# Kernel optimization log

Hardware: AMD Instinct MI355X
Metric: run time of the kernel (lower is better)

Reference implementation:

```python
import jax, jax.numpy as jnp
import numpy as np

N_EMB = 1024
N_HEAD = 16
HD = N_EMB // N_HEAD
ROPE_BASE = 10000.0


def _rope_cos_sin(seq_len, dim, dtype):
    inv_freq = 1.0 / (ROPE_BASE ** (jnp.arange(0, dim, 2, dtype=jnp.float32) / dim))
    t = jnp.arange(seq_len, dtype=jnp.float32)
    freqs = jnp.outer(t, inv_freq)              # [S, dim/2]
    emb = jnp.concatenate([freqs, freqs], -1)    # [S, dim]
    return jnp.cos(emb).astype(dtype), jnp.sin(emb).astype(dtype)


def _rotate_half(x):
    x1, x2 = jnp.split(x, 2, axis=-1)
    return jnp.concatenate([-x2, x1], axis=-1)


def _apply_rope(x):
    # x: [B, H, L, hd]; rotary over sequence axis (-2)
    cos, sin = _rope_cos_sin(x.shape[-2], x.shape[-1], x.dtype)
    return x * cos + _rotate_half(x) * sin


def setup_inputs() -> dict:
    key = jax.random.key(0)
    ks = jax.random.split(key, 8)
    B, T, S = 2, 2048, 2048
    std = 0.02
    return {
        "x": jax.random.normal(ks[0], (B, T, N_EMB), jnp.float32),
        "memory": jax.random.normal(ks[1], (B, S, N_EMB), jnp.float32),
        "q_w": jax.random.normal(ks[2], (N_EMB, N_EMB), jnp.float32) * std,
        "q_b": jnp.zeros((N_EMB,), jnp.float32),
        "kv_w": jax.random.normal(ks[3], (N_EMB, 2 * N_EMB), jnp.float32) * std,
        "kv_b": jnp.zeros((2 * N_EMB,), jnp.float32),
        "proj_w": jax.random.normal(ks[4], (N_EMB, N_EMB), jnp.float32) * std,
        "proj_b": jnp.zeros((N_EMB,), jnp.float32),
    }


def reference(x, memory, q_w, q_b, kv_w, kv_b, proj_w, proj_b):
    B, S, C = memory.shape
    T = x.shape[1]
    kv = memory @ kv_w + kv_b                      # [B,S,2C]
    K, V = jnp.split(kv, 2, axis=-1)
    Q = x @ q_w + q_b                              # [B,T,C]

    def heads(t, L):
        return t.reshape(B, L, N_HEAD, HD).transpose(0, 2, 1, 3)

    Q, K, V = heads(Q, T), heads(K, S), heads(V, S)
    Q = jax.nn.elu(Q) + 1.0                        # positive feature map
    K = jax.nn.elu(K) + 1.0
    Q_rot = _apply_rope(Q)
    K_rot = _apply_rope(K)
    # denom row-sum: sum_s Q.K_s == Q . (sum_s K_s) -- identical math, no SxT matrix
    denom = jnp.einsum('bhtd,bhd->bht', Q, K.sum(axis=2))[..., None]  # [B,H,T,1]
    att = jnp.einsum('bhtd,bhsd->bhts', Q_rot, K_rot) / denom          # [B,H,T,S]
    y = jnp.einsum('bhts,bhsd->bhtd', att, V)                          # [B,H,T,hd]
    y = y.transpose(0, 2, 1, 3).reshape(B, T, C)
    return y @ proj_w + proj_b
```

## Files before the change

kernel.cpp:

```cpp
#include <hip/hip_runtime.h>
#include <cstddef>
#include <cstdint>

#define B_SZ  2
#define T_SEQ 2048
#define S_SEQ 2048
#define C_EMB 1024
#define NH    16
#define HD    64
#define KDIM  1024

typedef __attribute__((ext_vector_type(8))) short bf16x8;
typedef __attribute__((ext_vector_type(4))) float f32x4;

#define OFF_XH    ((size_t)0)
#define OFF_XL    ((size_t)2097152)
#define OFF_MEMH  ((size_t)4194304)
#define OFF_MEML  ((size_t)6291456)
#define OFF_QWH   ((size_t)8388608)
#define OFF_QWL   ((size_t)8912896)
#define OFF_KVWH  ((size_t)9437184)
#define OFF_KVWL  ((size_t)10485760)
#define OFF_PWH   ((size_t)11534336)
#define OFF_PWL   ((size_t)12058624)
#define OFF_KSUM  ((size_t)12582912)
#define OFF_MT    ((size_t)12584960)
#define OFF_TAB   ((size_t)12716032)
#define OFF_YH    ((size_t)12847104)
#define OFF_YL    ((size_t)14944256)
#define WS_FLOATS ((size_t)17041408)

__device__ __forceinline__ float elu1(float v) {
    return v > 0.0f ? v + 1.0f : __expf(v);
}
__device__ __forceinline__ unsigned short bf16_rne(float x) {
    union { float f; unsigned int u; } v; v.f = x;
    unsigned int u = v.u;
    return (unsigned short)((u + 0x7FFFu + ((u >> 16) & 1u)) >> 16);
}
__device__ __forceinline__ float bf16_to_f(unsigned short h) {
    union { unsigned int u; float f; } v; v.u = ((unsigned int)h) << 16;
    return v.f;
}

#define PREP_BLOCKS 13064

__device__ __forceinline__ void split4_body(
    const float4* __restrict__ in, ushort4* __restrict__ hi,
    ushort4* __restrict__ lo, int i)
{
    float4 v = in[i];
    ushort4 h, l;
    h.x = bf16_rne(v.x); l.x = bf16_rne(v.x - bf16_to_f(h.x));
    h.y = bf16_rne(v.y); l.y = bf16_rne(v.y - bf16_to_f(h.y));
    h.z = bf16_rne(v.z); l.z = bf16_rne(v.z - bf16_to_f(h.z));
    h.w = bf16_rne(v.w); l.w = bf16_rne(v.w - bf16_to_f(h.w));
    hi[i] = h; lo[i] = l;
}

__device__ __forceinline__ void transpose_body(
    const float* __restrict__ W, unsigned short* __restrict__ Wth,
    unsigned short* __restrict__ Wtl, int K, int N, int bx, int by,
    float (*tile)[33])
{
    const int k0 = by * 32, n0 = bx * 32;
    const int tx = threadIdx.x & 31, ty = threadIdx.x >> 5;
    #pragma unroll
    for (int j = 0; j < 4; ++j)
        tile[ty + j * 8][tx] = W[(size_t)(k0 + ty + j * 8) * N + n0 + tx];
    __syncthreads();
    #pragma unroll
    for (int j = 0; j < 4; ++j) {
        float x = tile[tx][ty + j * 8];
        unsigned short h = bf16_rne(x);
        unsigned short l = bf16_rne(x - bf16_to_f(h));
        size_t o = (size_t)(n0 + ty + j * 8) * K + k0 + tx;
        Wth[o] = h; Wtl[o] = l;
    }
}

__global__ __launch_bounds__(256) void prep_kernel(
    const float* __restrict__ x, const float* __restrict__ memory,
    const float* __restrict__ q_w, const float* __restrict__ kv_w,
    const float* __restrict__ proj_w,
    unsigned short* __restrict__ xh, unsigned short* __restrict__ xl,
    unsigned short* __restrict__ mh, unsigned short* __restrict__ ml,
    unsigned short* __restrict__ qwh, unsigned short* __restrict__ qwl,
    unsigned short* __restrict__ kvwh, unsigned short* __restrict__ kvwl,
    unsigned short* __restrict__ pwh, unsigned short* __restrict__ pwl,
    float2* __restrict__ tab, float* __restrict__ zero_base)
{
    __shared__ float tile[32][33];
    const int bid = blockIdx.x;
    const int tid = threadIdx.x;
    if (bid < 4096) {
        split4_body((const float4*)x, (ushort4*)xh, (ushort4*)xl, bid * 256 + tid);
    } else if (bid < 8192) {
        split4_body((const float4*)memory, (ushort4*)mh, (ushort4*)ml, (bid - 4096) * 256 + tid);
    } else if (bid < 9216) {
        int i = bid - 8192;
        transpose_body(q_w, qwh, qwl, 1024, 1024, i & 31, i >> 5, tile);
    } else if (bid < 11264) {
        int i = bid - 9216;
        transpose_body(kv_w, kvwh, kvwl, 1024, 2048, i & 63, i >> 6, tile);
    } else if (bid < 12288) {
        int i = bid - 11264;
        transpose_body(proj_w, pwh, pwl, 1024, 1024, i & 31, i >> 5, tile);
    } else if (bid < 12544) {
        int idx = (bid - 12288) * 256 + tid;
        int pos = idx >> 5, i = idx & 31;
        double invf = exp(-(double)i * (9.210340371976184 / 32.0));
        float arg = (float)((double)pos * invf);
        float sn, cs;
        sincosf(arg, &sn, &cs);
        tab[idx] = make_float2(cs, sn);
    } else {
        int idx = (bid - 12544) * 256 + tid;
        if (idx < 2048 + 131072) zero_base[idx] = 0.0f;
    }
}

#define WAITCNT_VM(N)   asm volatile("s_waitcnt vmcnt(" #N ")" ::: "memory")
#define WAITCNT_LGKM(N) asm volatile("s_waitcnt lgkmcnt(" #N ")" ::: "memory")
#define CBAR()          asm volatile("" ::: "memory")

__device__ __forceinline__ void xcd_swz16(int& bx, int& by) {
    int id = (int)(blockIdx.x + (blockIdx.y << 4));
    int x = id & 7, k = id >> 3;
    bx = k >> 1;
    by = x * 2 + (k & 1);
}
__device__ __forceinline__ void xcd_swz32(int& bx, int& by) {
    int id = (int)(blockIdx.x + (blockIdx.y << 4));
    int x = id & 7, k = id >> 3;
    bx = k >> 2;
    by = x * 4 + (k & 3);
}

__global__ __launch_bounds__(512, 2) void gemm_kv(
    const unsigned short* __restrict__ Ah, const unsigned short* __restrict__ Al,
    const unsigned short* __restrict__ Bth, const unsigned short* __restrict__ Btl,
    const float* __restrict__ bias, const float2* __restrict__ tab,
    float* __restrict__ Ksum, float* __restrict__ Mt)
{
    __shared__ alignas(16) unsigned short smem[67584];
    const int tid = threadIdx.x;
    const int w = tid >> 6, lane = tid & 63;
    const int wr = w >> 1, wc = w & 1;
    const int quad = lane >> 4, lrow = lane & 15;
    int h, mt;
    xcd_swz16(h, mt);
    const int m0 = mt * 256;
    const int n0 = h * 64;
    const int b  = m0 >> 11;
    const int tbase = (m0 & 2047) + wr * 64;
    const int bh_idx = b * NH + h;

    const int sr = tid >> 2;
    const int g  = (tid & 3) ^ ((tid >> 3) & 3);
    const unsigned short* gA0 = Ah + (size_t)(m0 + sr) * KDIM + g * 8;
    const unsigned short* gA1 = Ah + (size_t)(m0 + 128 + sr) * KDIM + g * 8;
    const unsigned short* gA2 = Al + (size_t)(m0 + sr) * KDIM + g * 8;
    const unsigned short* gA3 = Al + (size_t)(m0 + 128 + sr) * KDIM + g * 8;
    const size_t brow = (size_t)(n0 + sr) + (sr >= 64 ? (size_t)960 : 0);
    const unsigned short* gB0 = Bth + brow * KDIM + g * 8;
    const unsigned short* gB1 = Btl + brow * KDIM + g * 8;
    const int lA0 = w * 512;
    const int lA1 = 4096 + w * 512;
    const int lA2 = 8192 + w * 512;
    const int lA3 = 12288 + w * 512;
    const int lB0 = 16384 + w * 512;
    const int lB1 = 20480 + w * 512;

    auto STAGE = [&](unsigned short* buf, int k0) {
        __builtin_amdgcn_global_load_lds(
            (const __attribute__((address_space(1))) unsigned int*)(gA0 + k0),
            (__attribute__((address_space(3))) unsigned int*)(buf + lA0), 16, 0, 0);
        __builtin_amdgcn_global_load_lds(
            (const __attribute__((address_space(1))) unsigned int*)(gA1 + k0),
            (__attribute__((address_space(3))) unsigned int*)(buf + lA1), 16, 0, 0);
        __builtin_amdgcn_global_load_lds(
            (const __attribute__((address_space(1))) unsigned int*)(gA2 + k0),
            (__attribute__((address_space(3))) unsigned int*)(buf + lA2), 16, 0, 0);
        __builtin_amdgcn_global_load_lds(
            (const __attribute__((address_space(1))) unsigned int*)(gA3 + k0),
            (__attribute__((address_space(3))) unsigned int*)(buf + lA3), 16, 0, 0);
        __builtin_amdgcn_global_load_lds(
            (const __attribute__((address_space(1))) unsigned int*)(gB0 + k0),
            (__attribute__((address_space(3))) unsigned int*)(buf + lB0), 16, 0, 0);
        __builtin_amdgcn_global_load_lds(
            (const __attribute__((address_space(1))) unsigned int*)(gB1 + k0),
            (__attribute__((address_space(3))) unsigned int*)(buf + lB1), 16, 0, 0);
    };

    const int rowbase = wr * 64, colbase = wc * 64;
    const int sw = ((quad ^ ((lrow >> 1) & 3)) << 3);

    f32x4 acc[4][4] = {};
    bf16x8 ahA[4], alA[4], bhA[4], blA[4];
    bf16x8 ahB[4], alB[4], bhB[4], blB[4];

    auto KV_READ = [&](bf16x8 (&AH)[4], bf16x8 (&AL)[4],
                       bf16x8 (&BH)[4], bf16x8 (&BL)[4],
                       const unsigned short* _b) {
        #pragma unroll
        for (int it = 0; it < 4; ++it) {
            int off = (rowbase + it * 16 + lrow) * 32 + sw;
            AH[it] = *(const bf16x8*)&_b[off];
            AL[it] = *(const bf16x8*)&_b[8192 + off];
        }
        #pragma unroll
        for (int jt = 0; jt < 4; ++jt) {
            int boff = (colbase + jt * 16 + lrow) * 32 + sw;
            BH[jt] = *(const bf16x8*)&_b[16384 + boff];
            BL[jt] = *(const bf16x8*)&_b[20480 + boff];
        }
    };
    auto KV_MFMA = [&](bf16x8 (&AH)[4], bf16x8 (&AL)[4],
                       bf16x8 (&BH)[4], bf16x8 (&BL)[4]) {
        #pragma unroll
        for (int it = 0; it < 4; ++it)
            #pragma unroll
            for (int jt = 0; jt < 4; ++jt)
                acc[it][jt] = __builtin_amdgcn_mfma_f32_16x16x32_bf16(AH[it], BH[jt], acc[it][jt], 0, 0, 0);
        #pragma unroll
        for (int it = 0; it < 4; ++it)
            #pragma unroll
            for (int jt = 0; jt < 4; ++jt)
                acc[it][jt] = __builtin_amdgcn_mfma_f32_16x16x32_bf16(AH[it], BL[jt], acc[it][jt], 0, 0, 0);
        #pragma unroll
        for (int it = 0; it < 4; ++it)
            #pragma unroll
            for (int jt = 0; jt < 4; ++jt)
                acc[it][jt] = __builtin_amdgcn_mfma_f32_16x16x32_bf16(AL[it], BH[jt], acc[it][jt], 0, 0, 0);
    };

    unsigned short* buf0 = smem;
    unsigned short* buf1 = smem + 24576;

    STAGE(buf0, 0);
    STAGE(buf1, 32);
    WAITCNT_VM(6);
    __builtin_amdgcn_s_barrier();
    KV_READ(ahA, alA, bhA, blA, buf0);

    #pragma unroll 1
    for (int t = 0; t < 32; t += 2) {
        WAITCNT_VM(0);
        WAITCNT_LGKM(0);
        __builtin_amdgcn_sched_barrier(0);
        __builtin_amdgcn_s_barrier();
        __builtin_amdgcn_sched_barrier(0);
        if (t + 2 < 32) STAGE(buf0, (t + 2) * 32);
        KV_READ(ahB, alB, bhB, blB, buf1);
        __builtin_amdgcn_s_setprio(1);
        KV_MFMA(ahA, alA, bhA, blA);
        __builtin_amdgcn_s_setprio(0);

        WAITCNT_VM(0);
        WAITCNT_LGKM(0);
        __builtin_amdgcn_sched_barrier(0);
        __builtin_amdgcn_s_barrier();
        __builtin_amdgcn_sched_barrier(0);
        if (t + 3 < 32) STAGE(buf1, (t + 3) * 32);
        if (t + 2 < 32) KV_READ(ahA, alA, bhA, blA, buf0);
        __builtin_amdgcn_s_setprio(1);
        KV_MFMA(ahB, alB, bhB, blB);
        __builtin_amdgcn_s_setprio(0);
    }
    __syncthreads();

    const bool isK = (wc == 0);
    const int colg = (isK ? 0 : C_EMB) + h * 64;
    float bb[4];
    #pragma unroll
    for (int jt = 0; jt < 4; ++jt) bb[jt] = bias[colg + jt * 16 + lrow];
    #pragma unroll
    for (int it = 0; it < 4; ++it)
        #pragma unroll
        for (int jt = 0; jt < 4; ++jt)
            #pragma unroll
            for (int r = 0; r < 4; ++r) {
                float v = acc[it][jt][r] + bb[jt];
                acc[it][jt][r] = isK ? elu1(v) : v;
            }

    if (isK) {
        #pragma unroll
        for (int jt = 0; jt < 4; ++jt) {
            float p = 0.0f;
            #pragma unroll
            for (int it = 0; it < 4; ++it)
                #pragma unroll
                for (int r = 0; r < 4; ++r) p += acc[it][jt][r];
            p += __shfl_xor(p, 16);
            p += __shfl_xor(p, 32);
            if (quad == 0)
                atomicAdd(&Ksum[b * C_EMB + h * 64 + jt * 16 + lrow], p);
        }
        #pragma unroll
        for (int it = 0; it < 4; ++it)
            #pragma unroll
            for (int r = 0; r < 4; ++r) {
                int s = tbase + it * 16 + quad * 4 + r;
                float2 c0 = tab[s * 32 + lrow];
                float2 c1 = tab[s * 32 + 16 + lrow];
                float a0 = acc[it][0][r], a1 = acc[it][1][r];
                float a2 = acc[it][2][r], a3 = acc[it][3][r];
                acc[it][0][r] = a0 * c0.x - a2 * c0.y;
                acc[it][2][r] = a2 * c0.x + a0 * c0.y;
                acc[it][1][r] = a1 * c1.x - a3 * c1.y;
                acc[it][3][r] = a3 * c1.x + a1 * c1.y;
            }
    }

    unsigned short* Hd = smem + (isK ? 0 : 33792);
    unsigned short* Ld = Hd + 16896;
    #pragma unroll
    for (int jt = 0; jt < 4; ++jt) {
        int d = jt * 16 + lrow;
        #pragma unroll
        for (int it = 0; it < 4; ++it) {
            int t0loc = wr * 64 + it * 16 + quad * 4;
            ushort4 h4, l4;
            float v0 = acc[it][jt][0], v1 = acc[it][jt][1];
            float v2 = acc[it][jt][2], v3 = acc[it][jt][3];
            h4.x = bf16_rne(v0); l4.x = bf16_rne(v0 - bf16_to_f(h4.x));
            h4.y = bf16_rne(v1); l4.y = bf16_rne(v1 - bf16_to_f(h4.y));
            h4.z = bf16_rne(v2); l4.z = bf16_rne(v2 - bf16_to_f(h4.z));
            h4.w = bf16_rne(v3); l4.w = bf16_rne(v3 - bf16_to_f(h4.w));
            *(ushort4*)&Hd[d * 264 + t0loc] = h4;
            *(ushort4*)&Ld[d * 264 + t0loc] = l4;
        }
    }
    __syncthreads();

    {
        const unsigned short* KH = smem;
        const unsigned short* KL = smem + 16896;
        const unsigned short* VH = smem + 33792;
        const unsigned short* VL = smem + 50688;
        const int mrow = (w & 3) * 16 + lrow;
        const int thalf = w >> 2;
        f32x4 macc[4] = {};
        #pragma unroll
        for (int ks = 0; ks < 4; ++ks) {
            int kof = thalf * 128 + ks * 32 + quad * 8;
            bf16x8 vah = *(const bf16x8*)&VH[mrow * 264 + kof];
            bf16x8 val = *(const bf16x8*)&VL[mrow * 264 + kof];
            #pragma unroll
            for (int jt = 0; jt < 4; ++jt) {
                int nrow = jt * 16 + lrow;
                bf16x8 kbh = *(const bf16x8*)&KH[nrow * 264 + kof];
                bf16x8 kbl = *(const bf16x8*)&KL[nrow * 264 + kof];
                macc[jt] = __builtin_amdgcn_mfma_f32_16x16x32_bf16(vah, kbh, macc[jt], 0, 0, 0);
                macc[jt] = __builtin_amdgcn_mfma_f32_16x16x32_bf16(vah, kbl, macc[jt], 0, 0, 0);
                macc[jt] = __builtin_amdgcn_mfma_f32_16x16x32_bf16(val, kbh, macc[jt], 0, 0, 0);
            }
        }
        #pragma unroll
        for (int jt = 0; jt < 4; ++jt)
            #pragma unroll
            for (int r = 0; r < 4; ++r)
                atomicAdd(&Mt[((size_t)bh_idx * 64 + (w & 3) * 16 + quad * 4 + r) * 64 + jt * 16 + lrow],
                          macc[jt][r]);
    }
}

__device__ __forceinline__ void gemm_main_128(
    const unsigned short* __restrict__ Ah, const unsigned short* __restrict__ Al,
    const unsigned short* __restrict__ Bth, const unsigned short* __restrict__ Btl,
    unsigned short* lds, int m0, int n0, f32x4 (&acc)[2][4])
{
    const int tid = threadIdx.x;
    const int w = tid >> 6, lane = tid & 63;
    const int quad = lane >> 4, lrow = lane & 15;
    const int srow = lane >> 2;
    const int g  = (lane & 3) ^ ((lane >> 3) & 3);
    const int sw = ((quad ^ ((lrow >> 1) & 3)) << 3);

    const unsigned short* gA0 = Ah + (size_t)(m0 + w * 16 + srow) * KDIM + g * 8;
    const unsigned short* gA1 = Ah + (size_t)(m0 + 64 + w * 16 + srow) * KDIM + g * 8;
    const unsigned short* gA2 = Al + (size_t)(m0 + w * 16 + srow) * KDIM + g * 8;
    const unsigned short* gA3 = Al + (size_t)(m0 + 64 + w * 16 + srow) * KDIM + g * 8;
    const unsigned short* gB0 = Bth + (size_t)(n0 + w * 16 + srow) * KDIM + g * 8;
    const unsigned short* gB1 = Btl + (size_t)(n0 + w * 16 + srow) * KDIM + g * 8;
    const int lA0 = w * 512, lA1 = 2048 + w * 512;
    const int lA2 = 4096 + w * 512, lA3 = 6144 + w * 512;
    const int lB0 = 8192 + w * 512, lB1 = 10240 + w * 512;

    auto STAGE = [&](unsigned short* buf, int k0) {
        __builtin_amdgcn_global_load_lds(
            (const __attribute__((address_space(1))) unsigned int*)(gA0 + k0),
            (__attribute__((address_space(3))) unsigned int*)(buf + lA0), 16, 0, 0);
        __builtin_amdgcn_global_load_lds(
            (const __attribute__((address_space(1))) unsigned int*)(gA1 + k0),
            (__attribute__((address_space(3))) unsigned int*)(buf + lA1), 16, 0, 0);
        __builtin_amdgcn_global_load_lds(
            (const __attribute__((address_space(1))) unsigned int*)(gA2 + k0),
            (__attribute__((address_space(3))) unsigned int*)(buf + lA2), 16, 0, 0);
        __builtin_amdgcn_global_load_lds(
            (const __attribute__((address_space(1))) unsigned int*)(gA3 + k0),
            (__attribute__((address_space(3))) unsigned int*)(buf + lA3), 16, 0, 0);
        __builtin_amdgcn_global_load_lds(
            (const __attribute__((address_space(1))) unsigned int*)(gB0 + k0),
            (__attribute__((address_space(3))) unsigned int*)(buf + lB0), 16, 0, 0);
        __builtin_amdgcn_global_load_lds(
            (const __attribute__((address_space(1))) unsigned int*)(gB1 + k0),
            (__attribute__((address_space(3))) unsigned int*)(buf + lB1), 16, 0, 0);
    };

    STAGE(lds, 0);

    #pragma unroll 1
    for (int t = 0; t < 32; ++t) {
        unsigned short* cur = lds + (t & 1) * 12288;
        unsigned short* nxt = lds + ((t + 1) & 1) * 12288;
        WAITCNT_VM(0);
        __builtin_amdgcn_sched_barrier(0);
        __builtin_amdgcn_s_barrier();
        __builtin_amdgcn_sched_barrier(0);

        bf16x8 ah[2], al[2], bh[4], bl[4];
        #pragma unroll
        for (int it = 0; it < 2; ++it) {
            int off = (w * 32 + it * 16 + lrow) * 32 + sw;
            ah[it] = *(const bf16x8*)&cur[off];
            al[it] = *(const bf16x8*)&cur[4096 + off];
        }
        #pragma unroll
        for (int jt = 0; jt < 2; ++jt) {
            int boff = (jt * 16 + lrow) * 32 + sw;
            bh[jt] = *(const bf16x8*)&cur[8192 + boff];
            bl[jt] = *(const bf16x8*)&cur[10240 + boff];
        }
        CBAR();
        #pragma unroll
        for (int jt = 2; jt < 4; ++jt) {
            int boff = (jt * 16 + lrow) * 32 + sw;
            bh[jt] = *(const bf16x8*)&cur[8192 + boff];
            bl[jt] = *(const bf16x8*)&cur[10240 + boff];
        }
        if (t + 1 < 32) STAGE(nxt, (t + 1) * 32);

        WAITCNT_LGKM(4);
        __builtin_amdgcn_sched_barrier(0);
        __builtin_amdgcn_s_setprio(1);
        #pragma unroll
        for (int it = 0; it < 2; ++it)
            #pragma unroll
            for (int jt = 0; jt < 2; ++jt)
                acc[it][jt] = __builtin_amdgcn_mfma_f32_16x16x32_bf16(ah[it], bh[jt], acc[it][jt], 0, 0, 0);
        #pragma unroll
        for (int it = 0; it < 2; ++it)
            #pragma unroll
            for (int jt = 0; jt < 2; ++jt)
                acc[it][jt] = __builtin_amdgcn_mfma_f32_16x16x32_bf16(ah[it], bl[jt], acc[it][jt], 0, 0, 0);
        #pragma unroll
        for (int it = 0; it < 2; ++it)
            #pragma unroll
            for (int jt = 0; jt < 2; ++jt)
                acc[it][jt] = __builtin_amdgcn_mfma_f32_16x16x32_bf16(al[it], bh[jt], acc[it][jt], 0, 0, 0);

        WAITCNT_LGKM(0);
        __builtin_amdgcn_sched_barrier(0);
        #pragma unroll
        for (int it = 0; it < 2; ++it)
            #pragma unroll
            for (int jt = 2; jt < 4; ++jt)
                acc[it][jt] = __builtin_amdgcn_mfma_f32_16x16x32_bf16(ah[it], bh[jt], acc[it][jt], 0, 0, 0);
        #pragma unroll
        for (int it = 0; it < 2; ++it)
            #pragma unroll
            for (int jt = 2; jt < 4; ++jt)
                acc[it][jt] = __builtin_amdgcn_mfma_f32_16x16x32_bf16(ah[it], bl[jt], acc[it][jt], 0, 0, 0);
        #pragma unroll
        for (int it = 0; it < 2; ++it)
            #pragma unroll
            for (int jt = 2; jt < 4; ++jt)
                acc[it][jt] = __builtin_amdgcn_mfma_f32_16x16x32_bf16(al[it], bh[jt], acc[it][jt], 0, 0, 0);
        __builtin_amdgcn_s_setprio(0);
    }
    __syncthreads();
}

__global__ __launch_bounds__(256, 3) void gemm_q(
    const unsigned short* __restrict__ Ah, const unsigned short* __restrict__ Al,
    const unsigned short* __restrict__ Bth, const unsigned short* __restrict__ Btl,
    const float* __restrict__ bias, const float2* __restrict__ tab,
    const float* __restrict__ Ksum, const float* __restrict__ Mt,
    unsigned short* __restrict__ Yh, unsigned short* __restrict__ Yl)
{
    __shared__ alignas(16) unsigned short smem[24576];
    int h, mt;
    xcd_swz32(h, mt);
    const int m0 = mt * 128;
    f32x4 acc[2][4] = {};
    gemm_main_128(Ah, Al, Bth, Btl, smem, m0, h * 64, acc);

    const int tid = threadIdx.x;
    const int w = tid >> 6, lane = tid & 63;
    const int quad = lane >> 4, lrow = lane & 15;
    const int b = m0 >> 11;
    const int tbase = (m0 & 2047) + w * 32;
    const int bh = b * NH + h;

    float bb[4];
    #pragma unroll
    for (int jt = 0; jt < 4; ++jt) bb[jt] = bias[h * 64 + jt * 16 + lrow];
    #pragma unroll
    for (int it = 0; it < 2; ++it)
        #pragma unroll
        for (int jt = 0; jt < 4; ++jt)
            #pragma unroll
            for (int r = 0; r < 4; ++r)
                acc[it][jt][r] = elu1(acc[it][jt][r] + bb[jt]);

    float ks[4], den_reg[2][4];
    #pragma unroll
    for (int jt = 0; jt < 4; ++jt) ks[jt] = Ksum[b * C_EMB + h * 64 + jt * 16 + lrow];
    #pragma unroll
    for (int it = 0; it < 2; ++it)
        #pragma unroll
        for (int r = 0; r < 4; ++r) {
            float p = acc[it][0][r] * ks[0] + acc[it][1][r] * ks[1]
                    + acc[it][2][r] * ks[2] + acc[it][3][r] * ks[3];
            p += __shfl_xor(p, 1);
            p += __shfl_xor(p, 2);
            p += __shfl_xor(p, 4);
            p += __shfl_xor(p, 8);
            den_reg[it][r] = p;
        }

    #pragma unroll
    for (int it = 0; it < 2; ++it)
        #pragma unroll
        for (int r = 0; r < 4; ++r) {
            int s = tbase + it * 16 + quad * 4 + r;
            float2 c0 = tab[s * 32 + lrow];
            float2 c1 = tab[s * 32 + 16 + lrow];
            float a0 = acc[it][0][r], a1 = acc[it][1][r];
            float a2 = acc[it][2][r], a3 = acc[it][3][r];
            acc[it][0][r] = a0 * c0.x - a2 * c0.y;
            acc[it][2][r] = a2 * c0.x + a0 * c0.y;
            acc[it][1][r] = a1 * c1.x - a3 * c1.y;
            acc[it][3][r] = a3 * c1.x + a1 * c1.y;
        }

    unsigned short* QH = smem + w * 4608;
    unsigned short* QL = QH + 2304;
    #pragma unroll
    for (int it = 0; it < 2; ++it)
        #pragma unroll
        for (int jt = 0; jt < 4; ++jt)
            #pragma unroll
            for (int r = 0; r < 4; ++r) {
                int tloc = it * 16 + quad * 4 + r;
                int d = jt * 16 + lrow;
                float v = acc[it][jt][r];
                unsigned short hh = bf16_rne(v);
                QH[tloc * 72 + d] = hh;
                QL[tloc * 72 + d] = bf16_rne(v - bf16_to_f(hh));
            }

    f32x4 acc2[2][4] = {};
    #pragma unroll
    for (int kc = 0; kc < 2; ++kc) {
        bf16x8 mbh[4], mbl[4];
        #pragma unroll
        for (int jt2 = 0; jt2 < 4; ++jt2) {
            const float* mp = &Mt[((size_t)bh * 64 + jt2 * 16 + lrow) * 64 + kc * 32 + quad * 8];
            #pragma unroll
            for (int e = 0; e < 8; ++e) {
                float x = mp[e];
                unsigned short hh = bf16_rne(x);
                mbh[jt2][e] = (short)hh;
                mbl[jt2][e] = (short)bf16_rne(x - bf16_to_f(hh));
            }
        }
        #pragma unroll
        for (int it2 = 0; it2 < 2; ++it2) {
            int ro = (it2 * 16 + lrow) * 72 + kc * 32 + quad * 8;
            bf16x8 qh = *(const bf16x8*)&QH[ro];
            bf16x8 ql = *(const bf16x8*)&QL[ro];
            #pragma unroll
            for (int jt2 = 0; jt2 < 4; ++jt2) {
                acc2[it2][jt2] = __builtin_amdgcn_mfma_f32_16x16x32_bf16(qh, mbh[jt2], acc2[it2][jt2], 0, 0, 0);
                acc2[it2][jt2] = __builtin_amdgcn_mfma_f32_16x16x32_bf16(qh, mbl[jt2], acc2[it2][jt2], 0, 0, 0);
                acc2[it2][jt2] = __builtin_amdgcn_mfma_f32_16x16x32_bf16(ql, mbh[jt2], acc2[it2][jt2], 0, 0, 0);
            }
        }
    }

    #pragma unroll
    for (int it2 = 0; it2 < 2; ++it2)
        #pragma unroll
        for (int jt2 = 0; jt2 < 4; ++jt2)
            #pragma unroll
            for (int r = 0; r < 4; ++r) {
                float v = acc2[it2][jt2][r] / den_reg[it2][r];
                size_t o = ((size_t)(m0 + w * 32 + it2 * 16 + quad * 4 + r)) * C_EMB
                         + h * 64 + jt2 * 16 + lrow;
                unsigned short hh = bf16_rne(v);
                Yh[o] = hh;
                Yl[o] = bf16_rne(v - bf16_to_f(hh));
            }
}

__global__ __launch_bounds__(256, 3) void gemm_out(
    const unsigned short* __restrict__ Ah, const unsigned short* __restrict__ Al,
    const unsigned short* __restrict__ Bth, const unsigned short* __restrict__ Btl,
    const float* __restrict__ bias, float* __restrict__ out)
{
    __shared__ alignas(16) unsigned short smem[24576];
    int nt, mt;
    xcd_swz32(nt, mt);
    const int m0 = mt * 128, n0 = nt * 64;
    f32x4 acc[2][4] = {};
    gemm_main_128(Ah, Al, Bth, Btl, smem, m0, n0, acc);

    const int tid = threadIdx.x;
    const int w = tid >> 6, lane = tid & 63;
    const int quad = lane >> 4, lrow = lane & 15;

    #pragma unroll
    for (int jt = 0; jt < 4; ++jt) {
        int gc = n0 + jt * 16 + lrow;
        float bb = bias[gc];
        #pragma unroll
        for (int it = 0; it < 2; ++it) {
            int grb = m0 + w * 32 + it * 16 + quad * 4;
            #pragma unroll
            for (int r = 0; r < 4; ++r)
                out[(size_t)(grb + r) * C_EMB + gc] = acc[it][jt][r] + bb;
        }
    }
}

extern "C" void kernel_launch(void* const* d_in, const int* in_sizes, int n_in,
                              void* d_out, int out_size, void* d_ws, size_t ws_size,
                              hipStream_t stream)
{
    const float* x      = (const float*)d_in[0];
    const float* memory = (const float*)d_in[1];
    const float* q_w    = (const float*)d_in[2];
    const float* q_b    = (const float*)d_in[3];
    const float* kv_w   = (const float*)d_in[4];
    const float* kv_b   = (const float*)d_in[5];
    const float* proj_w = (const float*)d_in[6];
    const float* proj_b = (const float*)d_in[7];

    if (ws_size < WS_FLOATS * sizeof(float)) return;

    float* ws = (float*)d_ws;
    unsigned short* xh   = (unsigned short*)(ws + OFF_XH);
    unsigned short* xl   = (unsigned short*)(ws + OFF_XL);
    unsigned short* mh   = (unsigned short*)(ws + OFF_MEMH);
    unsigned short* ml   = (unsigned short*)(ws + OFF_MEML);
    unsigned short* qwh  = (unsigned short*)(ws + OFF_QWH);
    unsigned short* qwl  = (unsigned short*)(ws + OFF_QWL);
    unsigned short* kvwh = (unsigned short*)(ws + OFF_KVWH);
    unsigned short* kvwl = (unsigned short*)(ws + OFF_KVWL);
    unsigned short* pwh  = (unsigned short*)(ws + OFF_PWH);
    unsigned short* pwl  = (unsigned short*)(ws + OFF_PWL);
    unsigned short* Yh   = (unsigned short*)(ws + OFF_YH);
    unsigned short* Yl   = (unsigned short*)(ws + OFF_YL);
    float*  Ksum = ws + OFF_KSUM;
    float*  Mm   = ws + OFF_MT;
    float2* tab  = (float2*)(ws + OFF_TAB);

    prep_kernel<<<PREP_BLOCKS, 256, 0, stream>>>(
        x, memory, q_w, kv_w, proj_w,
        xh, xl, mh, ml, qwh, qwl, kvwh, kvwl, pwh, pwl,
        tab, Ksum );

    gemm_kv<<<dim3(16, 16), 512, 0, stream>>>(mh, ml, kvwh, kvwl, kv_b, tab, Ksum, Mm);
    gemm_q<<<dim3(16, 32), 256, 0, stream>>>(xh, xl, qwh, qwl, q_b, tab, Ksum, Mm, Yh, Yl);
    gemm_out<<<dim3(16, 32), 256, 0, stream>>>(Yh, Yl, pwh, pwl, proj_b, (float*)d_out);
}
```

Baseline: 242.9 us.

## Halve gemm_kv M-tile to 128 rows and restructure its double-buffered pipeline

Changes the KV projection kernel from 256-row to 128-row tiles, doubling the grid to 512 blocks and raising launch bounds to allow 4 blocks per CU with half the LDS. The K-loop is rewritten to a single-step double buffer that splits the B-fragment reads and MFMAs into two halves, with partial lgkm waits. The aim is better occupancy and CU coverage, at the cost of lower per-block data reuse and twice as many atomic adds into Ksum and Mt.

```diff
diff --git a/kernel.cpp b/kernel.cpp
--- a/kernel.cpp
+++ b/kernel.cpp
@@ -124,12 +124,6 @@
 #define WAITCNT_LGKM(N) asm volatile("s_waitcnt lgkmcnt(" #N ")" ::: "memory")
 #define CBAR()          asm volatile("" ::: "memory")
 
-__device__ __forceinline__ void xcd_swz16(int& bx, int& by) {
-    int id = (int)(blockIdx.x + (blockIdx.y << 4));
-    int x = id & 7, k = id >> 3;
-    bx = k >> 1;
-    by = x * 2 + (k & 1);
-}
 __device__ __forceinline__ void xcd_swz32(int& bx, int& by) {
     int id = (int)(blockIdx.x + (blockIdx.y << 4));
     int x = id & 7, k = id >> 3;
@@ -137,135 +131,127 @@
     by = x * 4 + (k & 3);
 }
 
-__global__ __launch_bounds__(512, 2) void gemm_kv(
+__global__ __launch_bounds__(512, 4) void gemm_kv(
     const unsigned short* __restrict__ Ah, const unsigned short* __restrict__ Al,
     const unsigned short* __restrict__ Bth, const unsigned short* __restrict__ Btl,
     const float* __restrict__ bias, const float2* __restrict__ tab,
     float* __restrict__ Ksum, float* __restrict__ Mt)
 {
-    __shared__ alignas(16) unsigned short smem[67584];
+    __shared__ alignas(16) unsigned short smem[34816];
     const int tid = threadIdx.x;
     const int w = tid >> 6, lane = tid & 63;
     const int wr = w >> 1, wc = w & 1;
     const int quad = lane >> 4, lrow = lane & 15;
     int h, mt;
-    xcd_swz16(h, mt);
-    const int m0 = mt * 256;
+    xcd_swz32(h, mt);
+    const int m0 = mt * 128;
     const int n0 = h * 64;
     const int b  = m0 >> 11;
-    const int tbase = (m0 & 2047) + wr * 64;
+    const int tbase = (m0 & 2047) + wr * 32;
     const int bh_idx = b * NH + h;
 
-    const int sr = tid >> 2;
-    const int g  = (tid & 3) ^ ((tid >> 3) & 3);
-    const unsigned short* gA0 = Ah + (size_t)(m0 + sr) * KDIM + g * 8;
-    const unsigned short* gA1 = Ah + (size_t)(m0 + 128 + sr) * KDIM + g * 8;
-    const unsigned short* gA2 = Al + (size_t)(m0 + sr) * KDIM + g * 8;
-    const unsigned short* gA3 = Al + (size_t)(m0 + 128 + sr) * KDIM + g * 8;
-    const size_t brow = (size_t)(n0 + sr) + (sr >= 64 ? (size_t)960 : 0);
-    const unsigned short* gB0 = Bth + brow * KDIM + g * 8;
-    const unsigned short* gB1 = Btl + brow * KDIM + g * 8;
-    const int lA0 = w * 512;
-    const int lA1 = 4096 + w * 512;
-    const int lA2 = 8192 + w * 512;
-    const int lA3 = 12288 + w * 512;
-    const int lB0 = 16384 + w * 512;
-    const int lB1 = 20480 + w * 512;
+    const int sr = lane >> 2;
+    const int g  = (lane & 3) ^ ((lane >> 3) & 3);
+    const int arow = w * 16 + sr;
+    const unsigned short* gAh = Ah + (size_t)(m0 + arow) * KDIM + g * 8;
+    const unsigned short* gAl = Al + (size_t)(m0 + arow) * KDIM + g * 8;
+    const size_t brow = (size_t)(n0 + arow) + ((w >= 4) ? (size_t)960 : 0);
+    const unsigned short* gBh = Bth + brow * KDIM + g * 8;
+    const unsigned short* gBl = Btl + brow * KDIM + g * 8;
+    const int lAh = w * 512;
+    const int lAl = 4096 + w * 512;
+    const int lBh = 8192 + w * 512;
+    const int lBl = 12288 + w * 512;
 
     auto STAGE = [&](unsigned short* buf, int k0) {
         __builtin_amdgcn_global_load_lds(
-            (const __attribute__((address_space(1))) unsigned int*)(gA0 + k0),
-            (__attribute__((address_space(3))) unsigned int*)(buf + lA0), 16, 0, 0);
-        __builtin_amdgcn_global_load_lds(
-            (const __attribute__((address_space(1))) unsigned int*)(gA1 + k0),
-            (__attribute__((address_space(3))) unsigned int*)(buf + lA1), 16, 0, 0);
-        __builtin_amdgcn_global_load_lds(
-            (const __attribute__((address_space(1))) unsigned int*)(gA2 + k0),
-            (__attribute__((address_space(3))) unsigned int*)(buf + lA2), 16, 0, 0);
-        __builtin_amdgcn_global_load_lds(
-            (const __attribute__((address_space(1))) unsigned int*)(gA3 + k0),
-            (__attribute__((address_space(3))) unsigned int*)(buf + lA3), 16, 0, 0);
-        __builtin_amdgcn_global_load_lds(
-            (const __attribute__((address_space(1))) unsigned int*)(gB0 + k0),
-            (__attribute__((address_space(3))) unsigned int*)(buf + lB0), 16, 0, 0);
-        __builtin_amdgcn_global_load_lds(
-            (const __attribute__((address_space(1))) unsigned int*)(gB1 + k0),
-            (__attribute__((address_space(3))) unsigned int*)(buf + lB1), 16, 0, 0);
+            (const __attribute__((address_space(1))) unsigned int*)(gAh + k0),
+            (__attribute__((address_space(3))) unsigned int*)(buf + lAh), 16, 0, 0);
+        __builtin_amdgcn_global_load_lds(
+            (const __attribute__((address_space(1))) unsigned int*)(gAl + k0),
+            (__attribute__((address_space(3))) unsigned int*)(buf + lAl), 16, 0, 0);
+        __builtin_amdgcn_global_load_lds(
+            (const __attribute__((address_space(1))) unsigned int*)(gBh + k0),
+            (__attribute__((address_space(3))) unsigned int*)(buf + lBh), 16, 0, 0);
+        __builtin_amdgcn_global_load_lds(
+            (const __attribute__((address_space(1))) unsigned int*)(gBl + k0),
+            (__attribute__((address_space(3))) unsigned int*)(buf + lBl), 16, 0, 0);
     };
 
-    const int rowbase = wr * 64, colbase = wc * 64;
+    const int rowbase = wr * 32, colbase = wc * 64;
     const int sw = ((quad ^ ((lrow >> 1) & 3)) << 3);
 
-    f32x4 acc[4][4] = {};
-    bf16x8 ahA[4], alA[4], bhA[4], blA[4];
-    bf16x8 ahB[4], alB[4], bhB[4], blB[4];
-
-    auto KV_READ = [&](bf16x8 (&AH)[4], bf16x8 (&AL)[4],
-                       bf16x8 (&BH)[4], bf16x8 (&BL)[4],
-                       const unsigned short* _b) {
-        #pragma unroll
-        for (int it = 0; it < 4; ++it) {
+    f32x4 acc[2][4] = {};
+
+    STAGE(smem, 0);
+
+    #pragma unroll 1
+    for (int t = 0; t < 32; ++t) {
+        unsigned short* cur = smem + (t & 1) * 16384;
+        unsigned short* nxt = smem + ((t + 1) & 1) * 16384;
+        WAITCNT_VM(0);
+        __builtin_amdgcn_sched_barrier(0);
+        __builtin_amdgcn_s_barrier();
+        __builtin_amdgcn_sched_barrier(0);
+
+        bf16x8 ah[2], al[2], bh[4], bl[4];
+        #pragma unroll
+        for (int it = 0; it < 2; ++it) {
             int off = (rowbase + it * 16 + lrow) * 32 + sw;
-            AH[it] = *(const bf16x8*)&_b[off];
-            AL[it] = *(const bf16x8*)&_b[8192 + off];
-        }
-        #pragma unroll
-        for (int jt = 0; jt < 4; ++jt) {
+            ah[it] = *(const bf16x8*)&cur[off];
+            al[it] = *(const bf16x8*)&cur[4096 + off];
+        }
+        #pragma unroll
+        for (int jt = 0; jt < 2; ++jt) {
             int boff = (colbase + jt * 16 + lrow) * 32 + sw;
-            BH[jt] = *(const bf16x8*)&_b[16384 + boff];
-            BL[jt] = *(const bf16x8*)&_b[20480 + boff];
-        }
-    };
-    auto KV_MFMA = [&](bf16x8 (&AH)[4], bf16x8 (&AL)[4],
-                       bf16x8 (&BH)[4], bf16x8 (&BL)[4]) {
-        #pragma unroll
-        for (int it = 0; it < 4; ++it)
-            #pragma unroll
-            for (int jt = 0; jt < 4; ++jt)
-                acc[it][jt] = __builtin_amdgcn_mfma_f32_16x16x32_bf16(AH[it], BH[jt], acc[it][jt], 0, 0, 0);
-        #pragma unroll
-        for (int it = 0; it < 4; ++it)
-            #pragma unroll
-            for (int jt = 0; jt < 4; ++jt)
-                acc[it][jt] = __builtin_amdgcn_mfma_f32_16x16x32_bf16(AH[it], BL[jt], acc[it][jt], 0, 0, 0);
-        #pragma unroll
-        for (int it = 0; it < 4; ++it)
-            #pragma unroll
-            for (int jt = 0; jt < 4; ++jt)
-                acc[it][jt] = __builtin_amdgcn_mfma_f32_16x16x32_bf16(AL[it], BH[jt], acc[it][jt], 0, 0, 0);
-    };
-
-    unsigned short* buf0 = smem;
-    unsigned short* buf1 = smem + 24576;
-
-    STAGE(buf0, 0);
-    STAGE(buf1, 32);
-    WAITCNT_VM(6);
-    __builtin_amdgcn_s_barrier();
-    KV_READ(ahA, alA, bhA, blA, buf0);
-
-    #pragma unroll 1
-    for (int t = 0; t < 32; t += 2) {
-        WAITCNT_VM(0);
+            bh[jt] = *(const bf16x8*)&cur[8192 + boff];
+            bl[jt] = *(const bf16x8*)&cur[12288 + boff];
+        }
+        CBAR();
+        #pragma unroll
+        for (int jt = 2; jt < 4; ++jt) {
+            int boff = (colbase + jt * 16 + lrow) * 32 + sw;
+            bh[jt] = *(const bf16x8*)&cur[8192 + boff];
+            bl[jt] = *(const bf16x8*)&cur[12288 + boff];
+        }
+        if (t + 1 < 32) STAGE(nxt, (t + 1) * 32);
+
+        WAITCNT_LGKM(4);
+        __builtin_amdgcn_sched_barrier(0);
+        __builtin_amdgcn_s_setprio(1);
+        #pragma unroll
+        for (int it = 0; it < 2; ++it)
+            #pragma unroll
+            for (int jt = 0; jt < 2; ++jt)
+                acc[it][jt] = __builtin_amdgcn_mfma_f32_16x16x32_bf16(ah[it], bh[jt], acc[it][jt], 0, 0, 0);
+        #pragma unroll
+        for (int it = 0; it < 2; ++it)
+            #pragma unroll
+            for (int jt = 0; jt < 2; ++jt)
+                acc[it][jt] = __builtin_amdgcn_mfma_f32_16x16x32_bf16(ah[it], bl[jt], acc[it][jt], 0, 0, 0);
+        #pragma unroll
+        for (int it = 0; it < 2; ++it)
+            #pragma unroll
+            for (int jt = 0; jt < 2; ++jt)
+                acc[it][jt] = __builtin_amdgcn_mfma_f32_16x16x32_bf16(al[it], bh[jt], acc[it][jt], 0, 0, 0);
+
         WAITCNT_LGKM(0);
         __builtin_amdgcn_sched_barrier(0);
-        __builtin_amdgcn_s_barrier();
-        __builtin_amdgcn_sched_barrier(0);
-        if (t + 2 < 32) STAGE(buf0, (t + 2) * 32);
-        KV_READ(ahB, alB, bhB, blB, buf1);
-        __builtin_amdgcn_s_setprio(1);
-        KV_MFMA(ahA, alA, bhA, blA);
-        __builtin_amdgcn_s_setprio(0);
-
-        WAITCNT_VM(0);
-        WAITCNT_LGKM(0);
-        __builtin_amdgcn_sched_barrier(0);
-        __builtin_amdgcn_s_barrier();
-        __builtin_amdgcn_sched_barrier(0);
-        if (t + 3 < 32) STAGE(buf1, (t + 3) * 32);
-        if (t + 2 < 32) KV_READ(ahA, alA, bhA, blA, buf0);
-        __builtin_amdgcn_s_setprio(1);
-        KV_MFMA(ahB, alB, bhB, blB);
+        #pragma unroll
+        for (int it = 0; it < 2; ++it)
+            #pragma unroll
+            for (int jt = 2; jt < 4; ++jt)
+                acc[it][jt] = __builtin_amdgcn_mfma_f32_16x16x32_bf16(ah[it], bh[jt], acc[it][jt], 0, 0, 0);
+        #pragma unroll
+        for (int it = 0; it < 2; ++it)
+            #pragma unroll
+            for (int jt = 2; jt < 4; ++jt)
+                acc[it][jt] = __builtin_amdgcn_mfma_f32_16x16x32_bf16(ah[it], bl[jt], acc[it][jt], 0, 0, 0);
+        #pragma unroll
+        for (int it = 0; it < 2; ++it)
+            #pragma unroll
+            for (int jt = 2; jt < 4; ++jt)
+                acc[it][jt] = __builtin_amdgcn_mfma_f32_16x16x32_bf16(al[it], bh[jt], acc[it][jt], 0, 0, 0);
         __builtin_amdgcn_s_setprio(0);
     }
     __syncthreads();
@@ -276,7 +262,7 @@
     #pragma unroll
     for (int jt = 0; jt < 4; ++jt) bb[jt] = bias[colg + jt * 16 + lrow];
     #pragma unroll
-    for (int it = 0; it < 4; ++it)
+    for (int it = 0; it < 2; ++it)
         #pragma unroll
         for (int jt = 0; jt < 4; ++jt)
             #pragma unroll
@@ -290,7 +276,7 @@
         for (int jt = 0; jt < 4; ++jt) {
             float p = 0.0f;
             #pragma unroll
-            for (int it = 0; it < 4; ++it)
+            for (int it = 0; it < 2; ++it)
                 #pragma unroll
                 for (int r = 0; r < 4; ++r) p += acc[it][jt][r];
             p += __shfl_xor(p, 16);
@@ -299,7 +285,7 @@
                 atomicAdd(&Ksum[b * C_EMB + h * 64 + jt * 16 + lrow], p);
         }
         #pragma unroll
-        for (int it = 0; it < 4; ++it)
+        for (int it = 0; it < 2; ++it)
             #pragma unroll
             for (int r = 0; r < 4; ++r) {
                 int s = tbase + it * 16 + quad * 4 + r;
@@ -314,14 +300,14 @@
             }
     }
 
-    unsigned short* Hd = smem + (isK ? 0 : 33792);
-    unsigned short* Ld = Hd + 16896;
+    unsigned short* Hd = smem + (isK ? 0 : 17408);
+    unsigned short* Ld = Hd + 8704;
     #pragma unroll
     for (int jt = 0; jt < 4; ++jt) {
         int d = jt * 16 + lrow;
         #pragma unroll
-        for (int it = 0; it < 4; ++it) {
-            int t0loc = wr * 64 + it * 16 + quad * 4;
+        for (int it = 0; it < 2; ++it) {
+            int t0loc = wr * 32 + it * 16 + quad * 4;
             ushort4 h4, l4;
             float v0 = acc[it][jt][0], v1 = acc[it][jt][1];
             float v2 = acc[it][jt][2], v3 = acc[it][jt][3];
@@ -329,30 +315,30 @@
             h4.y = bf16_rne(v1); l4.y = bf16_rne(v1 - bf16_to_f(h4.y));
             h4.z = bf16_rne(v2); l4.z = bf16_rne(v2 - bf16_to_f(h4.z));
             h4.w = bf16_rne(v3); l4.w = bf16_rne(v3 - bf16_to_f(h4.w));
-            *(ushort4*)&Hd[d * 264 + t0loc] = h4;
-            *(ushort4*)&Ld[d * 264 + t0loc] = l4;
+            *(ushort4*)&Hd[d * 136 + t0loc] = h4;
+            *(ushort4*)&Ld[d * 136 + t0loc] = l4;
         }
     }
     __syncthreads();
 
     {
         const unsigned short* KH = smem;
-        const unsigned short* KL = smem + 16896;
-        const unsigned short* VH = smem + 33792;
-        const unsigned short* VL = smem + 50688;
+        const unsigned short* KL = smem + 8704;
+        const unsigned short* VH = smem + 17408;
+        const unsigned short* VL = smem + 26112;
         const int mrow = (w & 3) * 16 + lrow;
         const int thalf = w >> 2;
         f32x4 macc[4] = {};
         #pragma unroll
-        for (int ks = 0; ks < 4; ++ks) {
-            int kof = thalf * 128 + ks * 32 + quad * 8;
-            bf16x8 vah = *(const bf16x8*)&VH[mrow * 264 + kof];
-            bf16x8 val = *(const bf16x8*)&VL[mrow * 264 + kof];
+        for (int ks = 0; ks < 2; ++ks) {
+            int kof = thalf * 64 + ks * 32 + quad * 8;
+            bf16x8 vah = *(const bf16x8*)&VH[mrow * 136 + kof];
+            bf16x8 val = *(const bf16x8*)&VL[mrow * 136 + kof];
             #pragma unroll
             for (int jt = 0; jt < 4; ++jt) {
                 int nrow = jt * 16 + lrow;
-                bf16x8 kbh = *(const bf16x8*)&KH[nrow * 264 + kof];
-                bf16x8 kbl = *(const bf16x8*)&KL[nrow * 264 + kof];
+                bf16x8 kbh = *(const bf16x8*)&KH[nrow * 136 + kof];
+                bf16x8 kbl = *(const bf16x8*)&KL[nrow * 136 + kof];
                 macc[jt] = __builtin_amdgcn_mfma_f32_16x16x32_bf16(vah, kbh, macc[jt], 0, 0, 0);
                 macc[jt] = __builtin_amdgcn_mfma_f32_16x16x32_bf16(vah, kbl, macc[jt], 0, 0, 0);
                 macc[jt] = __builtin_amdgcn_mfma_f32_16x16x32_bf16(val, kbh, macc[jt], 0, 0, 0);
@@ -674,7 +660,7 @@
         xh, xl, mh, ml, qwh, qwl, kvwh, kvwl, pwh, pwl,
         tab, Ksum );
 
-    gemm_kv<<<dim3(16, 16), 512, 0, stream>>>(mh, ml, kvwh, kvwl, kv_b, tab, Ksum, Mm);
+    gemm_kv<<<dim3(16, 32), 512, 0, stream>>>(mh, ml, kvwh, kvwl, kv_b, tab, Ksum, Mm);
     gemm_q<<<dim3(16, 32), 256, 0, stream>>>(xh, xl, qwh, qwl, q_b, tab, Ksum, Mm, Yh, Yl);
     gemm_out<<<dim3(16, 32), 256, 0, stream>>>(Yh, Yl, pwh, pwl, proj_b, (float*)d_out);
 }
```

Measured after the change: 234.1 us. -3.6%, faster.

## Switch KV GEMM to triple-buffered LDS pipeline with split MFMA waits

Applied to the files above, without the earlier changes.

Moves the KV projection GEMM main loop into a helper that uses three rotating LDS buffers instead of two register/LDS ping-pong halves. Each iteration waits only for the oldest global-to-LDS stage, issues the next stage two tiles ahead, and splits the LDS fragment reads so half of the MFMAs can start before all B fragments arrive. The intent is to overlap global loads, LDS reads and MFMA work more deeply and to drop the full vmcnt(0) waits. In exchange, LDS use grows (73728 shorts) and launch_bounds no longer requests 2 blocks per CU, which may lower occupancy.

```diff
diff --git a/kernel.cpp b/kernel.cpp
--- a/kernel.cpp
+++ b/kernel.cpp
@@ -137,32 +137,28 @@
     by = x * 4 + (k & 3);
 }
 
-__global__ __launch_bounds__(512, 2) void gemm_kv(
+__device__ __forceinline__ void gemm_pipe_kv(
     const unsigned short* __restrict__ Ah, const unsigned short* __restrict__ Al,
     const unsigned short* __restrict__ Bth, const unsigned short* __restrict__ Btl,
-    const float* __restrict__ bias, const float2* __restrict__ tab,
-    float* __restrict__ Ksum, float* __restrict__ Mt)
-{
-    __shared__ alignas(16) unsigned short smem[67584];
+    unsigned short* lds, int m0, int n0, f32x4 (&acc)[4][4])
+{
+    constexpr int BUFSZ = 24576;
+    constexpr int NT = KDIM / 32;
     const int tid = threadIdx.x;
     const int w = tid >> 6, lane = tid & 63;
-    const int wr = w >> 1, wc = w & 1;
     const int quad = lane >> 4, lrow = lane & 15;
-    int h, mt;
-    xcd_swz16(h, mt);
-    const int m0 = mt * 256;
-    const int n0 = h * 64;
-    const int b  = m0 >> 11;
-    const int tbase = (m0 & 2047) + wr * 64;
-    const int bh_idx = b * NH + h;
-
     const int sr = tid >> 2;
     const int g  = (tid & 3) ^ ((tid >> 3) & 3);
+    const int wr = w >> 1, wc = w & 1;
+    const int rowbase = wr * 64;
+    const int colbase = wc * 64;
+    const int sw = ((quad ^ ((lrow >> 1) & 3)) << 3);
+
     const unsigned short* gA0 = Ah + (size_t)(m0 + sr) * KDIM + g * 8;
     const unsigned short* gA1 = Ah + (size_t)(m0 + 128 + sr) * KDIM + g * 8;
     const unsigned short* gA2 = Al + (size_t)(m0 + sr) * KDIM + g * 8;
     const unsigned short* gA3 = Al + (size_t)(m0 + 128 + sr) * KDIM + g * 8;
-    const size_t brow = (size_t)(n0 + sr) + (sr >= 64 ? (size_t)960 : 0);
+    size_t brow = (size_t)(n0 + sr) + (sr >= 64 ? (size_t)960 : 0);
     const unsigned short* gB0 = Bth + brow * KDIM + g * 8;
     const unsigned short* gB1 = Btl + brow * KDIM + g * 8;
     const int lA0 = w * 512;
@@ -193,82 +189,106 @@
             (__attribute__((address_space(3))) unsigned int*)(buf + lB1), 16, 0, 0);
     };
 
-    const int rowbase = wr * 64, colbase = wc * 64;
-    const int sw = ((quad ^ ((lrow >> 1) & 3)) << 3);
-
-    f32x4 acc[4][4] = {};
-    bf16x8 ahA[4], alA[4], bhA[4], blA[4];
-    bf16x8 ahB[4], alB[4], bhB[4], blB[4];
-
-    auto KV_READ = [&](bf16x8 (&AH)[4], bf16x8 (&AL)[4],
-                       bf16x8 (&BH)[4], bf16x8 (&BL)[4],
-                       const unsigned short* _b) {
+    unsigned short* cur = lds;
+    unsigned short* nxt = lds + BUFSZ;
+    unsigned short* thr = lds + 2 * BUFSZ;
+    STAGE(cur, 0);
+    STAGE(nxt, 32);
+
+    #pragma unroll 1
+    for (int t = 0; t < NT; ++t) {
+        if (t == NT - 1) {
+            WAITCNT_VM(0);
+        } else {
+            WAITCNT_VM(6);
+        }
+        __builtin_amdgcn_s_barrier();
+
+        bf16x8 ah[4], al[4], bh[4], bl[4];
         #pragma unroll
         for (int it = 0; it < 4; ++it) {
             int off = (rowbase + it * 16 + lrow) * 32 + sw;
-            AH[it] = *(const bf16x8*)&_b[off];
-            AL[it] = *(const bf16x8*)&_b[8192 + off];
-        }
-        #pragma unroll
-        for (int jt = 0; jt < 4; ++jt) {
+            ah[it] = *(const bf16x8*)&cur[off];
+            al[it] = *(const bf16x8*)&cur[8192 + off];
+        }
+        #pragma unroll
+        for (int jt = 0; jt < 2; ++jt) {
             int boff = (colbase + jt * 16 + lrow) * 32 + sw;
-            BH[jt] = *(const bf16x8*)&_b[16384 + boff];
-            BL[jt] = *(const bf16x8*)&_b[20480 + boff];
-        }
-    };
-    auto KV_MFMA = [&](bf16x8 (&AH)[4], bf16x8 (&AL)[4],
-                       bf16x8 (&BH)[4], bf16x8 (&BL)[4]) {
+            bh[jt] = *(const bf16x8*)&cur[16384 + boff];
+            bl[jt] = *(const bf16x8*)&cur[20480 + boff];
+        }
+        CBAR();
+        #pragma unroll
+        for (int jt = 2; jt < 4; ++jt) {
+            int boff = (colbase + jt * 16 + lrow) * 32 + sw;
+            bh[jt] = *(const bf16x8*)&cur[16384 + boff];
+            bl[jt] = *(const bf16x8*)&cur[20480 + boff];
+        }
+        if (t + 2 < NT) STAGE(thr, (t + 2) * 32);
+
+        WAITCNT_LGKM(4);
+        __builtin_amdgcn_sched_barrier(0);
+        __builtin_amdgcn_s_setprio(1);
         #pragma unroll
         for (int it = 0; it < 4; ++it)
             #pragma unroll
-            for (int jt = 0; jt < 4; ++jt)
-                acc[it][jt] = __builtin_amdgcn_mfma_f32_16x16x32_bf16(AH[it], BH[jt], acc[it][jt], 0, 0, 0);
+            for (int jt = 0; jt < 2; ++jt)
+                acc[it][jt] = __builtin_amdgcn_mfma_f32_16x16x32_bf16(ah[it], bh[jt], acc[it][jt], 0, 0, 0);
         #pragma unroll
         for (int it = 0; it < 4; ++it)
             #pragma unroll
-            for (int jt = 0; jt < 4; ++jt)
-                acc[it][jt] = __builtin_amdgcn_mfma_f32_16x16x32_bf16(AH[it], BL[jt], acc[it][jt], 0, 0, 0);
+            for (int jt = 0; jt < 2; ++jt)
+                acc[it][jt] = __builtin_amdgcn_mfma_f32_16x16x32_bf16(ah[it], bl[jt], acc[it][jt], 0, 0, 0);
         #pragma unroll
         for (int it = 0; it < 4; ++it)
             #pragma unroll
-            for (int jt = 0; jt < 4; ++jt)
-                acc[it][jt] = __builtin_amdgcn_mfma_f32_16x16x32_bf16(AL[it], BH[jt], acc[it][jt], 0, 0, 0);
-    };
-
-    unsigned short* buf0 = smem;
-    unsigned short* buf1 = smem + 24576;
-
-    STAGE(buf0, 0);
-    STAGE(buf1, 32);
-    WAITCNT_VM(6);
-    __builtin_amdgcn_s_barrier();
-    KV_READ(ahA, alA, bhA, blA, buf0);
-
-    #pragma unroll 1
-    for (int t = 0; t < 32; t += 2) {
-        WAITCNT_VM(0);
+            for (int jt = 0; jt < 2; ++jt)
+                acc[it][jt] = __builtin_amdgcn_mfma_f32_16x16x32_bf16(al[it], bh[jt], acc[it][jt], 0, 0, 0);
+
         WAITCNT_LGKM(0);
         __builtin_amdgcn_sched_barrier(0);
-        __builtin_amdgcn_s_barrier();
-        __builtin_amdgcn_sched_barrier(0);
-        if (t + 2 < 32) STAGE(buf0, (t + 2) * 32);
-        KV_READ(ahB, alB, bhB, blB, buf1);
-        __builtin_amdgcn_s_setprio(1);
-        KV_MFMA(ahA, alA, bhA, blA);
+        #pragma unroll
+        for (int it = 0; it < 4; ++it)
+            #pragma unroll
+            for (int jt = 2; jt < 4; ++jt)
+                acc[it][jt] = __builtin_amdgcn_mfma_f32_16x16x32_bf16(ah[it], bh[jt], acc[it][jt], 0, 0, 0);
+        #pragma unroll
+        for (int it = 0; it < 4; ++it)
+            #pragma unroll
+            for (int jt = 2; jt < 4; ++jt)
+                acc[it][jt] = __builtin_amdgcn_mfma_f32_16x16x32_bf16(ah[it], bl[jt], acc[it][jt], 0, 0, 0);
+        #pragma unroll
+        for (int it = 0; it < 4; ++it)
+            #pragma unroll
+            for (int jt = 2; jt < 4; ++jt)
+                acc[it][jt] = __builtin_amdgcn_mfma_f32_16x16x32_bf16(al[it], bh[jt], acc[it][jt], 0, 0, 0);
         __builtin_amdgcn_s_setprio(0);
 
-        WAITCNT_VM(0);
-        WAITCNT_LGKM(0);
-        __builtin_amdgcn_sched_barrier(0);
-        __builtin_amdgcn_s_barrier();
-        __builtin_amdgcn_sched_barrier(0);
-        if (t + 3 < 32) STAGE(buf1, (t + 3) * 32);
-        if (t + 2 < 32) KV_READ(ahA, alA, bhA, blA, buf0);
-        __builtin_amdgcn_s_setprio(1);
-        KV_MFMA(ahB, alB, bhB, blB);
-        __builtin_amdgcn_s_setprio(0);
+        unsigned short* tmp = cur; cur = nxt; nxt = thr; thr = tmp;
     }
     __syncthreads();
+}
+
+__global__ __launch_bounds__(512) void gemm_kv(
+    const unsigned short* __restrict__ Ah, const unsigned short* __restrict__ Al,
+    const unsigned short* __restrict__ Bth, const unsigned short* __restrict__ Btl,
+    const float* __restrict__ bias, const float2* __restrict__ tab,
+    float* __restrict__ Ksum, float* __restrict__ Mt)
+{
+    __shared__ alignas(16) unsigned short smem[73728];
+    const int tid = threadIdx.x;
+    const int w = tid >> 6, lane = tid & 63;
+    const int wr = w >> 1, wc = w & 1;
+    const int quad = lane >> 4, lrow = lane & 15;
+    int h, mt;
+    xcd_swz16(h, mt);
+    const int m0 = mt * 256;
+    const int b  = m0 >> 11;
+    const int tbase = (m0 & 2047) + wr * 64;
+    const int bh_idx = b * NH + h;
+
+    f32x4 acc[4][4] = {};
+    gemm_pipe_kv(Ah, Al, Bth, Btl, smem, m0, h * 64, acc);
 
     const bool isK = (wc == 0);
     const int colg = (isK ? 0 : C_EMB) + h * 64;
```

After: 226.2 us. -6.9%, faster.
